# Kernel optimization log

Measured on AMD Instinct MI355X. Metric: run time of the kernel, lower is better.

Reference implementation:

```python
import jax, jax.numpy as jnp
import numpy as np

WS = 8        # window_size
SHIFT = 4     # shift_size
HEADS = 3
DIM = 96
EPS = 1e-5

# static relative coordinates for one window (matches torch.meshgrid default 'ij')
_coords = np.stack(np.meshgrid(np.arange(WS), np.arange(WS), indexing='ij'))  # [2,ws,ws]
_flat = _coords.reshape(2, -1)                                               # [2,N]
_rel = _flat[:, :, None] - _flat[:, None, :]                                  # [2,N,N]
REL_ABS_SUM = jnp.asarray(np.abs(_rel[0]) + np.abs(_rel[1]), dtype=np.float32)  # [N,N]


def _layernorm(x, g, b):
    m = jnp.mean(x, axis=-1, keepdims=True)
    v = jnp.mean((x - m) ** 2, axis=-1, keepdims=True)
    return (x - m) * jax.lax.rsqrt(v + EPS) * g + b


def _band_shift(x, s):
    # x: [B,C,H,W]. Each band of WS rows: even band index -> roll +s along W, odd -> roll -s.
    B, C, H, W = x.shape
    xb = x.reshape(B, C, H // WS, WS, W)
    ev = jnp.roll(xb, s, axis=-1)
    od = jnp.roll(xb, -s, axis=-1)
    parity = (jnp.arange(H // WS) % 2 == 1).reshape(1, 1, -1, 1, 1)
    return jnp.where(parity, od, ev).reshape(B, C, H, W)


def _window_partition(x):
    # [B,C,H,W] -> [B*nH*nW, WS*WS, C]
    B, C, H, W = x.shape
    x = x.reshape(B, C, H // WS, WS, W // WS, WS)
    x = x.transpose(0, 2, 4, 3, 5, 1)
    return x.reshape(-1, WS * WS, C)


def _window_reverse(w, B, H, W, C):
    # [B*nH*nW, WS*WS, C] -> [B,C,H,W]
    x = w.reshape(B, H // WS, W // WS, WS, WS, C)
    x = x.transpose(0, 5, 1, 3, 2, 4)
    return x.reshape(B, C, H, W)


def setup_inputs() -> dict:
    key = jax.random.key(0)
    ks = jax.random.split(key, 8)
    d = DIM
    return {
        'x': jax.random.normal(ks[0], (2, d, 512, 512), jnp.float32),
        'ln1_g': jnp.ones((d,), jnp.float32),
        'ln1_b': jnp.zeros((d,), jnp.float32),
        'qkv_w': jax.random.normal(ks[1], (3 * d, d), jnp.float32) * 0.02,
        'qkv_b': jnp.zeros((3 * d,), jnp.float32),
        'lap_A': jnp.float32(1.0),
        'lap_B': jnp.float32(1.0),
        'proj_w': jax.random.normal(ks[2], (d, d), jnp.float32) * 0.02,
        'proj_b': jnp.zeros((d,), jnp.float32),
        'ln2_g': jnp.ones((d,), jnp.float32),
        'ln2_b': jnp.zeros((d,), jnp.float32),
        'mlp_w1': jax.random.normal(ks[3], (4 * d, d), jnp.float32) * 0.02,
        'mlp_b1': jnp.zeros((4 * d,), jnp.float32),
        'mlp_w2': jax.random.normal(ks[4], (d, 4 * d), jnp.float32) * 0.02,
        'mlp_b2': jnp.zeros((d,), jnp.float32),
    }


def reference(x, ln1_g, ln1_b, qkv_w, qkv_b, lap_A, lap_B, proj_w, proj_b,
              ln2_g, ln2_b, mlp_w1, mlp_b1, mlp_w2, mlp_b2):
    B, C, H, W = x.shape
    hd = C // HEADS
    scale = hd ** -0.5

    tokens = x.transpose(0, 2, 3, 1).reshape(B, H * W, C)  # [B,HW,C]
    shortcut = tokens
    xn = _layernorm(tokens, ln1_g, ln1_b)
    xn = xn.reshape(B, H, W, C).transpose(0, 3, 1, 2)       # [B,C,H,W]

    xs = _band_shift(xn, SHIFT)
    win = _window_partition(xs)                             # [Bw, N, C]

    # window attention
    Bw, N, _ = win.shape
    qkv = win @ qkv_w.T + qkv_b                             # [Bw,N,3C]
    qkv = qkv.reshape(Bw, N, 3, HEADS, hd)
    q = qkv[:, :, 0].transpose(0, 2, 1, 3) * scale          # [Bw,h,N,hd]
    k = qkv[:, :, 1].transpose(0, 2, 1, 3)
    v = qkv[:, :, 2].transpose(0, 2, 1, 3)
    attn = jnp.einsum('bhnd,bhmd->bhnm', q, k)              # [Bw,h,N,N]
    bias = (lap_A ** 2) * jnp.exp(-0.5 * (REL_ABS_SUM / (lap_B ** 2)))  # [N,N]
    attn = jax.nn.softmax(attn + bias[None, None], axis=-1)
    out = jnp.einsum('bhnm,bhmd->bhnd', attn, v)            # [Bw,h,N,hd]
    out = out.transpose(0, 2, 1, 3).reshape(Bw, N, C)
    out = out @ proj_w.T + proj_b

    xr = _window_reverse(out, B, H, W, C)                   # [B,C,H,W]
    xr = _band_shift(xr, -SHIFT)                            # inverse shift

    xt = xr.transpose(0, 2, 3, 1).reshape(B, H * W, C)
    xt = shortcut + xt
    h1 = _layernorm(xt, ln2_g, ln2_b)
    h1 = jax.nn.gelu(h1 @ mlp_w1.T + mlp_b1, approximate=False)
    xt = xt + (h1 @ mlp_w2.T + mlp_b2)

    return xt.reshape(B, H, W, C).transpose(0, 3, 1, 2)
```

## Files before the change

### kernel.cpp

```cpp
#include <hip/hip_runtime.h>
#include <hip/hip_bf16.h>

#define SHIFT 4

typedef short bf16x8 __attribute__((ext_vector_type(8)));
typedef float f32x4  __attribute__((ext_vector_type(4)));

#define MFMA(a, b, c) __builtin_amdgcn_mfma_f32_16x16x32_bf16((a), (b), (c), 0, 0, 0)

__device__ __forceinline__ unsigned short f2bf(float f) {
  __hip_bfloat16 h = __float2bfloat16(f);
  return __hip_bfloat16_raw(h).x;
}
__device__ __forceinline__ float bf2f(unsigned short u) {
  return __uint_as_float(((unsigned int)u) << 16);
}
template <int CTRL>
__device__ __forceinline__ float rr_add(float s) {
  int t = __builtin_amdgcn_update_dpp(0, __float_as_int(s), CTRL, 0xF, 0xF, false);
  return s + __uint_as_float(t);
}
__device__ __forceinline__ float rowsum16(float s) {
  s = rr_add<0x121>(s);
  s = rr_add<0x122>(s);
  s = rr_add<0x124>(s);
  s = rr_add<0x128>(s);
  return s;
}

__global__ void k_cvt_pt(const float* __restrict__ s, unsigned short* __restrict__ d, int n) {
  int i = blockIdx.x * 256 + threadIdx.x;
  if (i < n) {
    int col = i / 96, k = i - col * 96;
    d[(((col >> 4) * 3 + (k >> 5)) << 9) + ((col & 15) << 5) + (k & 31)] = f2bf(s[i]);
  }
}
__global__ void k_cvt_p2(const float* __restrict__ s, unsigned short* __restrict__ d) {
  int i = blockIdx.x * 256 + threadIdx.x;
  if (i < 36864) {
    int col = i / 384, k = i - col * 384;
    d[(((col >> 4) * 12 + (k >> 5)) << 9) + ((col & 15) << 5) + (k & 31)] = f2bf(s[i]);
  }
}

__global__ __launch_bounds__(256, 8) void k_pre(
    const float* __restrict__ x, unsigned short* __restrict__ X)
{
  __shared__ __align__(16) unsigned short xls[64 * 104];
  const int tid = threadIdx.x;
  const int bid = blockIdx.x;
  const int b  = bid >> 12;
  const int h  = (bid >> 3) & 511;
  const int w0 = (bid & 7) << 6;

#pragma unroll
  for (int v = 0; v < 6; ++v) {
    int idx4 = v * 256 + tid;
    int c    = idx4 >> 4;
    int p4   = (idx4 & 15) << 2;
    const float4 f = *reinterpret_cast<const float4*>(
        &x[((size_t)(b * 96 + c) << 18) + (h << 9) + w0 + p4]);
    xls[(p4 + 0) * 104 + c] = f2bf(f.x);
    xls[(p4 + 1) * 104 + c] = f2bf(f.y);
    xls[(p4 + 2) * 104 + c] = f2bf(f.z);
    xls[(p4 + 3) * 104 + c] = f2bf(f.w);
  }
  __syncthreads();
  const int q = tid & 3, t = tid >> 2;
  unsigned short* Xo = &X[(size_t)((b << 18) + (h << 9) + w0 + t) * 96 + q * 24];
#pragma unroll
  for (int v = 0; v < 3; ++v)
    *reinterpret_cast<bf16x8*>(&Xo[v * 8]) =
        *reinterpret_cast<const bf16x8*>(&xls[t * 104 + q * 24 + v * 8]);
}

__global__ __launch_bounds__(512, 1) void k_attn(
    const float* __restrict__ ln1g, const float* __restrict__ ln1b,
    const unsigned short* __restrict__ qkvwp,
    const float* __restrict__ qkvb,
    const float* __restrict__ lapA, const float* __restrict__ lapB,
    const unsigned short* __restrict__ projwp,
    const float* __restrict__ projb,
    unsigned short* __restrict__ X)
{
  __shared__ __align__(16) unsigned short WqkvL[27648];
  __shared__ __align__(16) unsigned short WprojL[9216];
  __shared__ __align__(16) unsigned short R1s[2][6656];
  __shared__ __align__(16) unsigned short Kss[2][6656];
  __shared__ __align__(16) unsigned short Vts[2][6912];

  const int tid  = threadIdx.x;
  const int lane = tid & 63;
  const int wv8  = tid >> 6;
  const int g    = wv8 >> 2;
  const int wvg  = wv8 & 3;
  const int l16  = lane & 15;
  const int lg   = lane >> 4;
  const int arow = wvg * 16 + l16;
  const f32x4 zz = {0.f, 0.f, 0.f, 0.f};

  unsigned short* R1 = R1s[g];
  unsigned short* Ks = Kss[g];
  unsigned short* Vt = Vts[g];

#pragma unroll
  for (int it = 0; it < 7; ++it) {
    int v8 = it * 512 + tid;
    if (v8 < 3456)
      *reinterpret_cast<bf16x8*>(&WqkvL[v8 * 8]) =
          *reinterpret_cast<const bf16x8*>(&qkvwp[v8 * 8]);
  }
#pragma unroll
  for (int it = 0; it < 3; ++it) {
    int v8 = it * 512 + tid;
    if (v8 < 1152)
      *reinterpret_cast<bf16x8*>(&WprojL[v8 * 8]) =
          *reinterpret_cast<const bf16x8*>(&projwp[v8 * 8]);
  }

  float gl[24], bl[24];
#pragma unroll
  for (int i = 0; i < 24; ++i) {
    int c = (i >> 3) * 32 + lg * 8 + (i & 7);
    gl[i] = ln1g[c]; bl[i] = ln1b[c];
  }
  float qb[18];
#pragma unroll
  for (int nt = 0; nt < 18; ++nt) qb[nt] = qkvb[nt * 16 + l16];
  float pbr[6];
#pragma unroll
  for (int nt = 0; nt < 6; ++nt) pbr[nt] = projb[nt * 16 + l16];

  float bias_r[4][4];
  {
    const float a = lapA[0], bb = lapB[0];
    const float A2 = a * a;
    const float nh = -0.5f / (bb * bb);
#pragma unroll
    for (int j = 0; j < 4; ++j) {
      int qi = wvg * 16 + lg * 4 + j;
      int qr = qi >> 3, qc = qi & 7;
#pragma unroll
      for (int kt = 0; kt < 4; ++kt) {
        int key = kt * 16 + l16;
        int dd = abs(qr - (key >> 3)) + abs(qc - (key & 7));
        bias_r[j][kt] = A2 * __expf(nh * (float)dd);
      }
    }
  }
  __syncthreads();

  const float qscale = 0.17677669529663687f;
  const int ftok = wvg * 16 + l16;

  auto xaddr = [&](int w) -> unsigned short* {
    int b  = w >> 12;
    int hi = (w >> 6) & 63;
    int wi = w & 63;
    int sh = ((hi & 1) == 0) ? -SHIFT : SHIFT;
    int fhh = hi * 8 + (ftok >> 3);
    int fww = ((wi * 8 + (ftok & 7)) + sh) & 511;
    return &X[(size_t)((b << 18) + (fhh << 9) + fww) * 96 + lg * 8];
  };

  int w = blockIdx.x * 32 + g;
  unsigned short* xfp = xaddr(w);
  bf16x8 xn[3];
#pragma unroll
  for (int ks = 0; ks < 3; ++ks)
    xn[ks] = *reinterpret_cast<const bf16x8*>(&xfp[ks * 32]);

#pragma unroll 1
  for (int it = 0; it < 16; ++it) {
    bf16x8 xc[3] = {xn[0], xn[1], xn[2]};

    float mu, rs;
    {
      float s1 = 0.f, s2 = 0.f;
#pragma unroll
      for (int ks = 0; ks < 3; ++ks)
#pragma unroll
        for (int e = 0; e < 8; ++e) {
          float v = bf2f((unsigned short)xc[ks][e]);
          s1 += v; s2 += v * v;
        }
      s1 += __shfl_xor(s1, 16); s2 += __shfl_xor(s2, 16);
      s1 += __shfl_xor(s1, 32); s2 += __shfl_xor(s2, 32);
      mu = s1 * (1.f / 96.f);
      rs = rsqrtf(s2 * (1.f / 96.f) - mu * mu + 1e-5f);
    }
    bf16x8 afr[3];
#pragma unroll
    for (int ks = 0; ks < 3; ++ks)
#pragma unroll
      for (int e = 0; e < 8; ++e)
        afr[ks][e] = (short)f2bf((bf2f((unsigned short)xc[ks][e]) - mu) * rs *
                                     gl[ks * 8 + e] + bl[ks * 8 + e]);

#pragma unroll
    for (int nt = 0; nt < 18; ++nt) {
      f32x4 acc = zz;
#pragma unroll
      for (int ks = 0; ks < 3; ++ks)
        acc = MFMA(afr[ks],
                   *reinterpret_cast<const bf16x8*>(&WqkvL[((nt * 3 + ks) << 9) + (l16 << 5) + lg * 8]),
                   acc);
      float bc = qb[nt];
      if (nt < 6) {
#pragma unroll
        for (int j = 0; j < 4; ++j)
          R1[(wvg * 16 + lg * 4 + j) * 104 + nt * 16 + l16] = f2bf((acc[j] + bc) * qscale);
      } else if (nt < 12) {
#pragma unroll
        for (int j = 0; j < 4; ++j)
          Ks[(wvg * 16 + lg * 4 + j) * 104 + (nt - 6) * 16 + l16] = f2bf(acc[j] + bc);
      } else {
#pragma unroll
        for (int j = 0; j < 4; ++j)
          Vt[((nt - 12) * 16 + l16) * 72 + wvg * 16 + lg * 4 + j] = f2bf(acc[j] + bc);
      }
    }
    __syncthreads();

    int wn = w + 2;
    if (wn > 8191) wn = w;
    unsigned short* xfpn = xaddr(wn);
#pragma unroll
    for (int ks = 0; ks < 3; ++ks)
      xn[ks] = *reinterpret_cast<const bf16x8*>(&xfpn[ks * 32]);

    bf16x8 aqh[3];
#pragma unroll
    for (int h = 0; h < 3; ++h)
      aqh[h] = *reinterpret_cast<const bf16x8*>(&R1[arow * 104 + h * 32 + lg * 8]);

    f32x4 oacc[6];
#pragma unroll
    for (int i = 0; i < 6; ++i) oacc[i] = zz;

#pragma unroll 1
    for (int h = 0; h < 3; ++h) {
      f32x4 sc[4];
#pragma unroll
      for (int kt = 0; kt < 4; ++kt) {
        bf16x8 bk = *reinterpret_cast<const bf16x8*>(&Ks[(kt * 16 + l16) * 104 + h * 32 + lg * 8]);
        sc[kt] = MFMA(aqh[h], bk, zz);
      }
#pragma unroll
      for (int j = 0; j < 4; ++j) {
        int qi = wvg * 16 + lg * 4 + j;
        float e0 = __expf(sc[0][j] + bias_r[j][0]);
        float e1 = __expf(sc[1][j] + bias_r[j][1]);
        float e2 = __expf(sc[2][j] + bias_r[j][2]);
        float e3 = __expf(sc[3][j] + bias_r[j][3]);
        float s = rowsum16(e0 + e1 + e2 + e3);
        float inv = __builtin_amdgcn_rcpf(s);
        R1[qi * 104 +  0 + l16] = f2bf(e0 * inv);
        R1[qi * 104 + 16 + l16] = f2bf(e1 * inv);
        R1[qi * 104 + 32 + l16] = f2bf(e2 * inv);
        R1[qi * 104 + 48 + l16] = f2bf(e3 * inv);
      }
      bf16x8 ap0 = *reinterpret_cast<const bf16x8*>(&R1[arow * 104 +  0 + lg * 8]);
      bf16x8 ap1 = *reinterpret_cast<const bf16x8*>(&R1[arow * 104 + 32 + lg * 8]);
#pragma unroll
      for (int dt = 0; dt < 2; ++dt) {
        int vcol = h * 32 + dt * 16 + l16;
        bf16x8 bv0 = *reinterpret_cast<const bf16x8*>(&Vt[vcol * 72 +  0 + lg * 8]);
        bf16x8 bv1 = *reinterpret_cast<const bf16x8*>(&Vt[vcol * 72 + 32 + lg * 8]);
        oacc[h * 2 + dt] = MFMA(ap0, bv0, oacc[h * 2 + dt]);
        oacc[h * 2 + dt] = MFMA(ap1, bv1, oacc[h * 2 + dt]);
      }
    }
    __syncthreads();

#pragma unroll
    for (int i = 0; i < 6; ++i)
#pragma unroll
      for (int j = 0; j < 4; ++j)
        R1[(wvg * 16 + lg * 4 + j) * 104 + i * 16 + l16] = f2bf(oacc[i][j]);

    bf16x8 ao[3];
#pragma unroll
    for (int ks = 0; ks < 3; ++ks)
      ao[ks] = *reinterpret_cast<const bf16x8*>(&R1[arow * 104 + ks * 32 + lg * 8]);
#pragma unroll
    for (int nt = 0; nt < 6; ++nt) {
      f32x4 acc = zz;
#pragma unroll
      for (int ks = 0; ks < 3; ++ks)
        acc = MFMA(ao[ks],
                   *reinterpret_cast<const bf16x8*>(&WprojL[((nt * 3 + ks) << 9) + (l16 << 5) + lg * 8]),
                   acc);
      float pb = pbr[nt];
#pragma unroll
      for (int j = 0; j < 4; ++j)
        R1[(wvg * 16 + lg * 4 + j) * 104 + nt * 16 + l16] = f2bf(acc[j] + pb);
    }
#pragma unroll
    for (int ks = 0; ks < 3; ++ks) {
      bf16x8 m = *reinterpret_cast<const bf16x8*>(&R1[ftok * 104 + ks * 32 + lg * 8]);
      bf16x8 pk;
#pragma unroll
      for (int e = 0; e < 8; ++e)
        pk[e] = (short)f2bf(bf2f((unsigned short)m[e]) + bf2f((unsigned short)xc[ks][e]));
      *reinterpret_cast<bf16x8*>(&xfp[ks * 32]) = pk;
    }
    xfp = xfpn;
    w = wn;
  }
}

__global__ __launch_bounds__(512, 2) void k_mlp(
    const unsigned short* __restrict__ X,
    const float* __restrict__ ln2g, const float* __restrict__ ln2b,
    const unsigned short* __restrict__ w1p,
    const float* __restrict__ b1,
    const unsigned short* __restrict__ w2p,
    const float* __restrict__ b2,
    float* __restrict__ out)
{
  __shared__ __align__(16) unsigned short Wl[36864];
  __shared__ __align__(16) unsigned short W2l[34816];
  __shared__ __align__(16) unsigned short Hl[128 * 72];

  const int tid = threadIdx.x;
  const int q    = tid & 3;
  const int t    = tid >> 2;
  const int lane = tid & 63;
  const int wv   = tid >> 6;
  const int l16  = lane & 15;
  const int lg   = lane >> 4;
  const f32x4 zz = {0.f, 0.f, 0.f, 0.f};

#pragma unroll
  for (int it = 0; it < 9; ++it) {
    int v8 = it * 512 + tid;
    *reinterpret_cast<bf16x8*>(&Wl[v8 * 8]) = *reinterpret_cast<const bf16x8*>(&w1p[v8 * 8]);
    if (v8 < 4352)
      *reinterpret_cast<bf16x8*>(&W2l[v8 * 8]) = *reinterpret_cast<const bf16x8*>(&w2p[v8 * 8]);
  }
  bf16x8 wfr[4];
#pragma unroll
  for (int r = 0; r < 4; ++r)
    wfr[r] = *reinterpret_cast<const bf16x8*>(&w2p[((68 + r) << 9) + (l16 << 5) + lg * 8]);

  float gr[24], br[24], b1r[24], b2r[6];
#pragma unroll
  for (int i = 0; i < 24; ++i) {
    int c = (i >> 3) * 32 + lg * 8 + (i & 7);
    gr[i] = ln2g[c]; br[i] = ln2b[c];
  }
#pragma unroll
  for (int i = 0; i < 24; ++i) b1r[i] = b1[i * 16 + l16];
#pragma unroll
  for (int i = 0; i < 6; ++i) b2r[i] = b2[i * 16 + l16];

  __syncthreads();

#pragma unroll 1
  for (int s = 0; s < 8; ++s) {
    const int stb = (blockIdx.x * 8 + s) * 128;

    const unsigned short* xfp = &X[(size_t)(stb + wv * 16 + l16) * 96 + lg * 8];
    float xv[24];
#pragma unroll
    for (int ks = 0; ks < 3; ++ks) {
      bf16x8 g2 = *reinterpret_cast<const bf16x8*>(&xfp[ks * 32]);
#pragma unroll
      for (int e = 0; e < 8; ++e) xv[ks * 8 + e] = bf2f((unsigned short)g2[e]);
    }
    float mu, rs;
    {
      float s1 = 0.f, s2 = 0.f;
#pragma unroll
      for (int k = 0; k < 24; ++k) { float v = xv[k]; s1 += v; s2 += v * v; }
      s1 += __shfl_xor(s1, 16); s2 += __shfl_xor(s2, 16);
      s1 += __shfl_xor(s1, 32); s2 += __shfl_xor(s2, 32);
      mu = s1 * (1.f / 96.f);
      rs = rsqrtf(s2 * (1.f / 96.f) - mu * mu + 1e-5f);
    }
    bf16x8 a1[3];
#pragma unroll
    for (int ks = 0; ks < 3; ++ks)
#pragma unroll
      for (int e = 0; e < 8; ++e)
        a1[ks][e] = (short)f2bf((xv[ks * 8 + e] - mu) * rs * gr[ks * 8 + e] + br[ks * 8 + e]);

    f32x4 acc2[6];
#pragma unroll
    for (int i = 0; i < 6; ++i) acc2[i] = zz;

#pragma unroll
    for (int ch = 0; ch < 6; ++ch) {
#pragma unroll
      for (int nt = 0; nt < 4; ++nt) {
        const int ntg = ch * 4 + nt;
        f32x4 acc = zz;
#pragma unroll
        for (int ks = 0; ks < 3; ++ks)
          acc = MFMA(a1[ks],
                     *reinterpret_cast<const bf16x8*>(&Wl[((ntg * 3 + ks) << 9) + (l16 << 5) + lg * 8]),
                     acc);
        float bb = b1r[ntg];
#pragma unroll
        for (int j = 0; j < 4; ++j) {
          float v = acc[j] + bb;
          float tt = v * fmaf(0.071354816f, v * v, 1.5957691f);
          float gg = v * __builtin_amdgcn_rcpf(1.f + __expf(-tt));
          Hl[(wv * 16 + lg * 4 + j) * 72 + nt * 16 + l16] = f2bf(gg);
        }
      }
      bf16x8 ah0 = *reinterpret_cast<const bf16x8*>(&Hl[(wv * 16 + l16) * 72 + lg * 8]);
      bf16x8 ah1 = *reinterpret_cast<const bf16x8*>(&Hl[(wv * 16 + l16) * 72 + 32 + lg * 8]);
#pragma unroll
      for (int nt = 0; nt < 6; ++nt) {
        const int t0 = nt * 12 + ch * 2;
        const int t1 = t0 + 1;
        bf16x8 bf0 = (t0 >= 68) ? wfr[(t0 - 68) & 3]
                   : *reinterpret_cast<const bf16x8*>(&W2l[(t0 << 9) + (l16 << 5) + lg * 8]);
        bf16x8 bf1 = (t1 >= 68) ? wfr[(t1 - 68) & 3]
                   : *reinterpret_cast<const bf16x8*>(&W2l[(t1 << 9) + (l16 << 5) + lg * 8]);
        acc2[nt] = MFMA(ah0, bf0, acc2[nt]);
        acc2[nt] = MFMA(ah1, bf1, acc2[nt]);
      }
    }

    const int tok = stb + t;
    const unsigned short* xrp = &X[(size_t)tok * 96 + q * 24];
    const int bb_ = tok >> 18;
    const int pix = tok & 262143;
#pragma unroll
    for (int pass = 0; pass < 2; ++pass) {
#pragma unroll
      for (int ntl = 0; ntl < 3; ++ntl) {
        const int nt = pass * 3 + ntl;
#pragma unroll
        for (int j = 0; j < 4; ++j)
          Hl[(wv * 16 + lg * 4 + j) * 72 + ntl * 16 + l16] = f2bf(acc2[nt][j] + b2r[nt]);
      }
      if ((q >> 1) == pass) {
        const int lc = (q & 1) * 24;
#pragma unroll
        for (int v = 0; v < 3; ++v) {
          bf16x8 m  = *reinterpret_cast<const bf16x8*>(&Hl[t * 72 + lc + v * 8]);
          bf16x8 xr = *reinterpret_cast<const bf16x8*>(&xrp[v * 8]);
#pragma unroll
          for (int e = 0; e < 8; ++e) {
            int c = q * 24 + v * 8 + e;
            out[((size_t)(bb_ * 96 + c) << 18) + pix] =
                bf2f((unsigned short)m[e]) + bf2f((unsigned short)xr[e]);
          }
        }
      }
    }
  }
}

extern "C" void kernel_launch(void* const* d_in, const int* in_sizes, int n_in,
                              void* d_out, int out_size, void* d_ws, size_t ws_size,
                              hipStream_t stream) {
  const float* x     = (const float*)d_in[0];
  const float* ln1g  = (const float*)d_in[1];
  const float* ln1b  = (const float*)d_in[2];
  const float* qkv_w = (const float*)d_in[3];
  const float* qkv_b = (const float*)d_in[4];
  const float* lapA  = (const float*)d_in[5];
  const float* lapB  = (const float*)d_in[6];
  const float* prj_w = (const float*)d_in[7];
  const float* prj_b = (const float*)d_in[8];
  const float* ln2g  = (const float*)d_in[9];
  const float* ln2b  = (const float*)d_in[10];
  const float* w1f   = (const float*)d_in[11];
  const float* b1    = (const float*)d_in[12];
  const float* w2f   = (const float*)d_in[13];
  const float* b2    = (const float*)d_in[14];

  char* ws = (char*)d_ws;
  unsigned short* X     = (unsigned short*)ws;
  unsigned short* qkvwp = (unsigned short*)(ws + 100663296);
  unsigned short* prjwp = (unsigned short*)(ws + 100718592);
  unsigned short* w1p   = (unsigned short*)(ws + 100737024);
  unsigned short* w2p   = (unsigned short*)(ws + 100810752);

  k_cvt_pt<<<108, 256, 0, stream>>>(qkv_w, qkvwp, 288 * 96);
  k_cvt_pt<<<36,  256, 0, stream>>>(prj_w, prjwp, 96 * 96);
  k_cvt_pt<<<144, 256, 0, stream>>>(w1f,   w1p,   384 * 96);
  k_cvt_p2<<<144, 256, 0, stream>>>(w2f, w2p);

  k_pre <<<8192, 256, 0, stream>>>(x, X);
  k_attn<<<256, 512, 0, stream>>>(ln1g, ln1b, qkvwp, qkv_b, lapA, lapB,
                                  prjwp, prj_b, X);
  k_mlp <<<512, 512, 0, stream>>>(X, ln2g, ln2b, w1p, b1, w2p, b2,
                                  (float*)d_out);
}
```

Before: 471.6 us.

## Run MLP kernel as 1024-thread blocks sharing one LDS weight copy

Reshapes k_mlp from 512-thread blocks into 1024-thread blocks. Each block holds two 8-wave groups that share a single LDS copy of the MLP weights, and each group has its own hidden-activation buffer and processes 4 of the block's 8 token tiles. The second weight matrix is only partly staged in LDS: tiles 51 and up are read from global memory through a scalar-held pointer. The LayerNorm gamma and beta are kept as packed bf16 in registers to cut register pressure. The goal is more resident waves per CU within the LDS budget. The cost is extra global/L2 traffic for the unstaged weight tiles and a small precision change in the LayerNorm affine parameters.

```diff
diff --git a/kernel.cpp b/kernel.cpp
--- a/kernel.cpp
+++ b/kernel.cpp
@@ -310,7 +310,7 @@
   }
 }
 
-__global__ __launch_bounds__(512, 2) void k_mlp(
+__global__ __launch_bounds__(1024, 1) void k_mlp(
     const unsigned short* __restrict__ X,
     const float* __restrict__ ln2g, const float* __restrict__ ln2b,
     const unsigned short* __restrict__ w1p,
@@ -320,23 +320,32 @@
     float* __restrict__ out)
 {
   __shared__ __align__(16) unsigned short Wl[36864];
-  __shared__ __align__(16) unsigned short W2l[34816];
-  __shared__ __align__(16) unsigned short Hl[128 * 72];
-
-  const int tid = threadIdx.x;
-  const int q    = tid & 3;
-  const int t    = tid >> 2;
+  __shared__ __align__(16) unsigned short W2l[26112];
+  __shared__ __align__(16) unsigned short Hl[2][9216];
+
+  const int tid  = threadIdx.x;
   const int lane = tid & 63;
-  const int wv   = tid >> 6;
+  const int wv16 = tid >> 6;
+  const int grp  = wv16 >> 3;
+  const int gwv  = wv16 & 7;
   const int l16  = lane & 15;
   const int lg   = lane >> 4;
+  const int gtid = tid & 511;
+  const int q    = gtid & 3;
+  const int t    = gtid >> 2;
   const f32x4 zz = {0.f, 0.f, 0.f, 0.f};
-
-#pragma unroll
-  for (int it = 0; it < 9; ++it) {
-    int v8 = it * 512 + tid;
-    *reinterpret_cast<bf16x8*>(&Wl[v8 * 8]) = *reinterpret_cast<const bf16x8*>(&w1p[v8 * 8]);
-    if (v8 < 4352)
+  unsigned short* Hlg = Hl[grp];
+
+#pragma unroll
+  for (int it = 0; it < 5; ++it) {
+    int v8 = it * 1024 + tid;
+    if (v8 < 4608)
+      *reinterpret_cast<bf16x8*>(&Wl[v8 * 8]) = *reinterpret_cast<const bf16x8*>(&w1p[v8 * 8]);
+  }
+#pragma unroll
+  for (int it = 0; it < 4; ++it) {
+    int v8 = it * 1024 + tid;
+    if (v8 < 3264)
       *reinterpret_cast<bf16x8*>(&W2l[v8 * 8]) = *reinterpret_cast<const bf16x8*>(&w2p[v8 * 8]);
   }
   bf16x8 wfr[4];
@@ -344,12 +353,16 @@
   for (int r = 0; r < 4; ++r)
     wfr[r] = *reinterpret_cast<const bf16x8*>(&w2p[((68 + r) << 9) + (l16 << 5) + lg * 8]);
 
-  float gr[24], br[24], b1r[24], b2r[6];
-#pragma unroll
-  for (int i = 0; i < 24; ++i) {
-    int c = (i >> 3) * 32 + lg * 8 + (i & 7);
-    gr[i] = ln2g[c]; br[i] = ln2b[c];
-  }
+  bf16x8 glb[3], blb[3];
+#pragma unroll
+  for (int ks = 0; ks < 3; ++ks)
+#pragma unroll
+    for (int e = 0; e < 8; ++e) {
+      int c = ks * 32 + lg * 8 + e;
+      glb[ks][e] = (short)f2bf(ln2g[c]);
+      blb[ks][e] = (short)f2bf(ln2b[c]);
+    }
+  float b1r[24], b2r[6];
 #pragma unroll
   for (int i = 0; i < 24; ++i) b1r[i] = b1[i * 16 + l16];
 #pragma unroll
@@ -358,10 +371,14 @@
   __syncthreads();
 
 #pragma unroll 1
-  for (int s = 0; s < 8; ++s) {
-    const int stb = (blockIdx.x * 8 + s) * 128;
-
-    const unsigned short* xfp = &X[(size_t)(stb + wv * 16 + l16) * 96 + lg * 8];
+  for (int s = 0; s < 4; ++s) {
+    unsigned long long wb = (unsigned long long)w2p;
+    asm volatile("" : "+s"(wb));
+    const unsigned short* w2sv = (const unsigned short*)wb;
+
+    const int stb = (blockIdx.x * 8 + grp * 4 + s) * 128;
+
+    const unsigned short* xfp = &X[(size_t)(stb + gwv * 16 + l16) * 96 + lg * 8];
     float xv[24];
 #pragma unroll
     for (int ks = 0; ks < 3; ++ks) {
@@ -384,7 +401,9 @@
     for (int ks = 0; ks < 3; ++ks)
 #pragma unroll
       for (int e = 0; e < 8; ++e)
-        a1[ks][e] = (short)f2bf((xv[ks * 8 + e] - mu) * rs * gr[ks * 8 + e] + br[ks * 8 + e]);
+        a1[ks][e] = (short)f2bf((xv[ks * 8 + e] - mu) * rs *
+                                    bf2f((unsigned short)glb[ks][e]) +
+                                bf2f((unsigned short)blb[ks][e]));
 
     f32x4 acc2[6];
 #pragma unroll
@@ -407,19 +426,23 @@
           float v = acc[j] + bb;
           float tt = v * fmaf(0.071354816f, v * v, 1.5957691f);
           float gg = v * __builtin_amdgcn_rcpf(1.f + __expf(-tt));
-          Hl[(wv * 16 + lg * 4 + j) * 72 + nt * 16 + l16] = f2bf(gg);
+          Hlg[(gwv * 16 + lg * 4 + j) * 72 + nt * 16 + l16] = f2bf(gg);
         }
       }
-      bf16x8 ah0 = *reinterpret_cast<const bf16x8*>(&Hl[(wv * 16 + l16) * 72 + lg * 8]);
-      bf16x8 ah1 = *reinterpret_cast<const bf16x8*>(&Hl[(wv * 16 + l16) * 72 + 32 + lg * 8]);
+      bf16x8 ah0 = *reinterpret_cast<const bf16x8*>(&Hlg[(gwv * 16 + l16) * 72 + lg * 8]);
+      bf16x8 ah1 = *reinterpret_cast<const bf16x8*>(&Hlg[(gwv * 16 + l16) * 72 + 32 + lg * 8]);
 #pragma unroll
       for (int nt = 0; nt < 6; ++nt) {
         const int t0 = nt * 12 + ch * 2;
         const int t1 = t0 + 1;
         bf16x8 bf0 = (t0 >= 68) ? wfr[(t0 - 68) & 3]
-                   : *reinterpret_cast<const bf16x8*>(&W2l[(t0 << 9) + (l16 << 5) + lg * 8]);
+                   : (t0 >= 51)
+                       ? *reinterpret_cast<const bf16x8*>(&w2sv[(t0 << 9) + (l16 << 5) + lg * 8])
+                       : *reinterpret_cast<const bf16x8*>(&W2l[(t0 << 9) + (l16 << 5) + lg * 8]);
         bf16x8 bf1 = (t1 >= 68) ? wfr[(t1 - 68) & 3]
-                   : *reinterpret_cast<const bf16x8*>(&W2l[(t1 << 9) + (l16 << 5) + lg * 8]);
+                   : (t1 >= 51)
+                       ? *reinterpret_cast<const bf16x8*>(&w2sv[(t1 << 9) + (l16 << 5) + lg * 8])
+                       : *reinterpret_cast<const bf16x8*>(&W2l[(t1 << 9) + (l16 << 5) + lg * 8]);
         acc2[nt] = MFMA(ah0, bf0, acc2[nt]);
         acc2[nt] = MFMA(ah1, bf1, acc2[nt]);
       }
@@ -436,13 +459,13 @@
         const int nt = pass * 3 + ntl;
 #pragma unroll
         for (int j = 0; j < 4; ++j)
-          Hl[(wv * 16 + lg * 4 + j) * 72 + ntl * 16 + l16] = f2bf(acc2[nt][j] + b2r[nt]);
+          Hlg[(gwv * 16 + lg * 4 + j) * 72 + ntl * 16 + l16] = f2bf(acc2[nt][j] + b2r[nt]);
       }
       if ((q >> 1) == pass) {
         const int lc = (q & 1) * 24;
 #pragma unroll
         for (int v = 0; v < 3; ++v) {
-          bf16x8 m  = *reinterpret_cast<const bf16x8*>(&Hl[t * 72 + lc + v * 8]);
+          bf16x8 m  = *reinterpret_cast<const bf16x8*>(&Hlg[t * 72 + lc + v * 8]);
           bf16x8 xr = *reinterpret_cast<const bf16x8*>(&xrp[v * 8]);
 #pragma unroll
           for (int e = 0; e < 8; ++e) {
@@ -490,6 +513,6 @@
   k_pre <<<8192, 256, 0, stream>>>(x, X);
   k_attn<<<256, 512, 0, stream>>>(ln1g, ln1b, qkvwp, qkv_b, lapA, lapB,
                                   prjwp, prj_b, X);
-  k_mlp <<<512, 512, 0, stream>>>(X, ln2g, ln2b, w1p, b1, w2p, b2,
-                                  (float*)d_out);
-}
+  k_mlp <<<512, 1024, 0, stream>>>(X, ln2g, ln2b, w1p, b1, w2p, b2,
+                                   (float*)d_out);
+}
```

Result: slower. 514.8 us (+9.2%).
